# Optimization experiments

Measured on AMD Instinct MI355X. Metric: run time of the kernel, lower is better.

## Reference

```python
import jax, jax.numpy as jnp
import numpy as np

BS, N, IN_F, OUT_F, HEADS = 32, 512, 256, 128, 4
NEG_SLOPE = 0.2


def setup_inputs() -> dict:
    key = jax.random.key(0)
    k1, k2, k3, k4, k5 = jax.random.split(key, 5)
    inputs = jax.random.normal(k1, (BS, N, IN_F), dtype=jnp.float32)
    adj = (jax.random.uniform(k2, (BS, N, N)) > 0.5).astype(jnp.float32)
    # xavier_normal-style init with relu gain sqrt(2)
    w = jax.random.normal(k3, (IN_F, HEADS * OUT_F), dtype=jnp.float32) * (
        np.sqrt(2.0) * np.sqrt(2.0 / (IN_F + HEADS * OUT_F))
    )
    a_i = jax.random.normal(k4, (HEADS, OUT_F, 1), dtype=jnp.float32) * (
        np.sqrt(2.0) * np.sqrt(2.0 / (OUT_F + 1))
    )
    a_j = jax.random.normal(k5, (HEADS, OUT_F, 1), dtype=jnp.float32) * (
        np.sqrt(2.0) * np.sqrt(2.0 / (OUT_F + 1))
    )
    bias = jnp.zeros((HEADS * OUT_F,), dtype=jnp.float32)
    return {"inputs": inputs, "adj": adj, "w": w, "a_i": a_i, "a_j": a_j, "bias": bias}


def reference(inputs, adj, w, a_i, a_j, bias):
    bs, n, _ = inputs.shape
    H, D = a_i.shape[0], a_i.shape[1]
    # self_loop_type == 2: adjacency unchanged
    # project: [bs, n, H, D]
    h = jnp.matmul(inputs, w).reshape(bs, n, H, D)
    # additive attention coefficients: [bs, n, H]
    coeff_i = jnp.einsum('bnhd,hdo->bnho', h, a_i)[..., 0]
    coeff_j = jnp.einsum('bnhd,hdo->bnho', h, a_j)[..., 0]
    # broadcast-sum scores e[b, i, j, h], leaky relu
    e = jax.nn.leaky_relu(coeff_i[:, :, None, :] + coeff_j[:, None, :, :],
                          negative_slope=NEG_SLOPE)
    adj_h = adj[..., None]  # [bs, n, n, 1], broadcasts over heads
    masked_e = jnp.where(adj_h <= 0, jnp.float32(-1e9), e)
    # softmax over neighbor axis j (dim 2), then re-mask
    attention = jax.nn.softmax(masked_e, axis=2) * adj_h
    # dropout = 0.0 -> no-op; normalize=False, average=False
    # per-head aggregation, all heads at once: out[b,i,h,d] = sum_j att[b,i,j,h] h[b,j,h,d]
    out = jnp.einsum('bijh,bjhd->bihd', attention, h).reshape(bs, n, H * D)
    return out + bias
```

## Files before the change

### kernel.cpp

```cpp
#include <hip/hip_runtime.h>

#define BSZ 32
#define NN 512
#define INF 256
#define NH 4
#define HD 512
#define NEG_SLOPE 0.2f

typedef __attribute__((ext_vector_type(8))) short bf16x8;
typedef __attribute__((ext_vector_type(8))) unsigned short ushort8;
typedef __attribute__((ext_vector_type(4))) float f32x4;

static __device__ __forceinline__ unsigned short f2bf(float f) {
    unsigned u = __builtin_bit_cast(unsigned, f);
    return (unsigned short)((u + 0x7FFFu + ((u >> 16) & 1u)) >> 16);
}

static __device__ __forceinline__ bf16x8 pk8(float4 a, float4 b) {
    unsigned d0, d1, d2, d3;
    asm("v_cvt_pk_bf16_f32 %0, %1, %2" : "=v"(d0) : "v"(a.x), "v"(a.y));
    asm("v_cvt_pk_bf16_f32 %0, %1, %2" : "=v"(d1) : "v"(a.z), "v"(a.w));
    asm("v_cvt_pk_bf16_f32 %0, %1, %2" : "=v"(d2) : "v"(b.x), "v"(b.y));
    asm("v_cvt_pk_bf16_f32 %0, %1, %2" : "=v"(d3) : "v"(b.z), "v"(b.w));
    uint4 u; u.x = d0; u.y = d1; u.z = d2; u.w = d3;
    return __builtin_bit_cast(bf16x8, u);
}

static __device__ __forceinline__ void gl_lds16(const void* g, void* l) {
    __builtin_amdgcn_global_load_lds(
        (const __attribute__((address_space(1))) unsigned int*)g,
        (__attribute__((address_space(3))) unsigned int*)l, 16, 0, 0);
}

__global__ __launch_bounds__(256) void k_prep(
    const float* __restrict__ w, unsigned short* __restrict__ wB,
    const float* __restrict__ adj, unsigned char* __restrict__ mbB)
{
    const int bid = blockIdx.x;
    if (bid < 2048) {
        const int swz = (bid & 7) * 256 + (bid >> 3);
        const int lane = threadIdx.x & 63, wave = threadIdx.x >> 6;
        const int row0 = swz * 8 + wave * 2;
        #pragma unroll
        for (int rr = 0; rr < 2; ++rr) {
            const float* ap = adj + (size_t)(row0 + rr) * NN + lane * 8;
            float4 a0 = *(const float4*)ap;
            float4 a1 = *(const float4*)(ap + 4);
            unsigned byte = 0;
            byte |= (a0.x > 0.f) ? 1u : 0u;  byte |= (a0.y > 0.f) ? 2u : 0u;
            byte |= (a0.z > 0.f) ? 4u : 0u;  byte |= (a0.w > 0.f) ? 8u : 0u;
            byte |= (a1.x > 0.f) ? 16u : 0u; byte |= (a1.y > 0.f) ? 32u : 0u;
            byte |= (a1.z > 0.f) ? 64u : 0u; byte |= (a1.w > 0.f) ? 128u : 0u;
            mbB[(size_t)(row0 + rr) * 64 + lane] = (unsigned char)byte;
        }
    } else {
        int gid = (bid - 2048) * 256 + threadIdx.x;
        int c = gid & 511, k = gid >> 9;
        int kb = k >> 5, g = (k >> 3) & 3, e = k & 7;
        wB[(((size_t)(kb * 4 + g) * 512) + c) * 8 + e] = f2bf(w[(size_t)k * 512 + c]);
    }
}

__global__ __launch_bounds__(256) void k_proj(
    const float* __restrict__ x, const unsigned short* __restrict__ wB,
    const float* __restrict__ ai, const float* __restrict__ aj,
    unsigned short* __restrict__ hB, float* __restrict__ ciT, float* __restrict__ cjT)
{
    __shared__ unsigned short hs[NH * 4096];
    const int tid = threadIdx.x;
    const int lane = tid & 63, head = tid >> 6;
    const int l15 = lane & 15, g = lane >> 4;
    const int orig = blockIdx.x;
    const int swz = (orig & 7) * 64 + (orig >> 3);
    const int row0 = swz * 32;

    f32x4 acc[2][8] = {};
    const float* xp0 = x + (size_t)(row0 + l15) * INF + g * 8;
    const float* xp1 = xp0 + 16 * INF;
    const unsigned short* bp = wB + ((size_t)g * 512 + head * 128 + l15) * 8;

    #pragma unroll
    for (int kb = 0; kb < 8; ++kb) {
        float4 f0 = *(const float4*)(xp0 + kb * 32);
        float4 f1 = *(const float4*)(xp0 + kb * 32 + 4);
        float4 f2 = *(const float4*)(xp1 + kb * 32);
        float4 f3 = *(const float4*)(xp1 + kb * 32 + 4);
        bf16x8 a0 = pk8(f0, f1);
        bf16x8 a1 = pk8(f2, f3);
        #pragma unroll
        for (int nf = 0; nf < 8; ++nf) {
            bf16x8 bv = *(const bf16x8*)(bp + (size_t)kb * 16384 + nf * 128);
            acc[0][nf] = __builtin_amdgcn_mfma_f32_16x16x32_bf16(a0, bv, acc[0][nf], 0, 0, 0);
            acc[1][nf] = __builtin_amdgcn_mfma_f32_16x16x32_bf16(a1, bv, acc[1][nf], 0, 0, 0);
        }
    }

    float aiv[8], ajv[8];
    #pragma unroll
    for (int nf = 0; nf < 8; ++nf) {
        aiv[nf] = ai[head * 128 + nf * 16 + l15];
        ajv[nf] = aj[head * 128 + nf * 16 + l15];
    }
    const int b = row0 >> 9;
    const int nloc0 = row0 & 511;
    const int kb2 = nloc0 >> 5;

    #pragma unroll
    for (int m = 0; m < 2; ++m) {
        float pi[4] = {0,0,0,0}, pj[4] = {0,0,0,0};
        #pragma unroll
        for (int nf = 0; nf < 8; ++nf)
            #pragma unroll
            for (int reg = 0; reg < 4; ++reg) {
                pi[reg] = fmaf(acc[m][nf][reg], aiv[nf], pi[reg]);
                pj[reg] = fmaf(acc[m][nf][reg], ajv[nf], pj[reg]);
            }
        #pragma unroll
        for (int reg = 0; reg < 4; ++reg) {
            #pragma unroll
            for (int off = 1; off < 16; off <<= 1) {
                pi[reg] += __shfl_xor(pi[reg], off);
                pj[reg] += __shfl_xor(pj[reg], off);
            }
        }
        if (l15 == 0) {
            #pragma unroll
            for (int reg = 0; reg < 4; ++reg) {
                int n = nloc0 + 16 * m + 4 * g + reg;
                ciT[((size_t)(head * BSZ + b) * NN) + n] = pi[reg];
                cjT[((size_t)(head * BSZ + b) * NN) + n] = pj[reg];
            }
        }
        #pragma unroll
        for (int reg = 0; reg < 4; ++reg) {
            int jloc = 16 * m + 4 * g + reg;
            int g2 = jloc >> 3, e = jloc & 7;
            #pragma unroll
            for (int nf = 0; nf < 8; ++nf)
                hs[head * 4096 + nf * 512 + g2 * 128 + l15 * 8 + e] =
                    f2bf(acc[m][nf][reg]);
        }
    }
    __syncthreads();
    {
        ushort8* dst = (ushort8*)(hB + (((size_t)(b * 4 + head) * 16 + kb2) * 4096));
        const ushort8* src = (const ushort8*)(hs + head * 4096);
        #pragma unroll
        for (int it = 0; it < 8; ++it)
            dst[it * 64 + lane] = src[it * 64 + lane];
    }
}

__global__ __launch_bounds__(256, 4) void k_attn(
    const unsigned short* __restrict__ hB, const float* __restrict__ ciT,
    const float* __restrict__ cjT, const unsigned* __restrict__ mb,
    const float* __restrict__ bias, float* __restrict__ out)
{
    __shared__ __align__(16) unsigned short Bst[2][4096];
    __shared__ __align__(16) float cjh[NN];
    __shared__ float cih[64];
    __shared__ unsigned maskS[64][17];
    __shared__ float Mpart[4];

    const int tid = threadIdx.x;
    const int lane = tid & 63, wave = tid >> 6;
    const int l15 = lane & 15, g = lane >> 4;

    const int orig = blockIdx.x;
    const int swz = (orig & 7) * 128 + (orig >> 3);
    const int b  = swz >> 5;
    const int h  = (swz >> 3) & 3;
    const int i0 = (swz & 7) * 64;

    const char* gslab = (const char*)(hB + (size_t)(b * NH + h) * 65536);

    gl_lds16(gslab + wave * 2048 + lane * 16,        (char*)&Bst[0][0] + wave * 2048);
    gl_lds16(gslab + wave * 2048 + 1024 + lane * 16, (char*)&Bst[0][0] + wave * 2048 + 1024);

    {
        const float* src = cjT + (size_t)(h * BSZ + b) * NN;
        float v0 = src[tid], v1 = src[tid + 256];
        cjh[tid] = v0; cjh[tid + 256] = v1;
        float mv = fmaxf(v0, v1);
        #pragma unroll
        for (int off = 32; off; off >>= 1) mv = fmaxf(mv, __shfl_xor(mv, off));
        if (lane == 0) Mpart[wave] = mv;
        if (tid < 64) cih[tid] = ciT[(size_t)(h * BSZ + b) * NN + i0 + tid];
        uint4 m4 = ((const uint4*)(mb + ((size_t)b * NN + i0) * 16))[tid];
        int base = tid * 4, row = base >> 4, wi = base & 15;
        maskS[row][wi] = m4.x; maskS[row][wi + 1] = m4.y;
        maskS[row][wi + 2] = m4.z; maskS[row][wi + 3] = m4.w;
    }
    __syncthreads();

    const float M = fmaxf(fmaxf(Mpart[0], Mpart[1]), fmaxf(Mpart[2], Mpart[3]));
    const float bc = cih[wave * 16 + l15];
    float smx = bc + M;
    const float mrow = fmaxf(smx, NEG_SLOPE * smx);

    float bvv[8];
    #pragma unroll
    for (int nf = 0; nf < 8; ++nf) bvv[nf] = bias[h * 128 + nf * 16 + l15];

    bf16x8 ones;
    #pragma unroll
    for (int e = 0; e < 8; ++e) ones[e] = (short)0x3F80;

    f32x4 acc[8] = {};
    f32x4 accs = {};
    int cur = 0;
    const unsigned* mrowp = maskS[wave * 16 + l15];

    for (int kb = 0; kb < 16; ++kb) {
        if (kb < 15) {
            const char* gs = gslab + (size_t)(kb + 1) * 8192 + wave * 2048 + lane * 16;
            char* ld = (char*)&Bst[cur ^ 1][0] + wave * 2048;
            gl_lds16(gs, ld);
            gl_lds16(gs + 1024, ld + 1024);
        }

        float4 cva = *(const float4*)&cjh[kb * 32 + g * 8];
        float4 cvb = *(const float4*)&cjh[kb * 32 + g * 8 + 4];
        float cj8[8] = {cva.x, cva.y, cva.z, cva.w, cvb.x, cvb.y, cvb.z, cvb.w};
        unsigned byte = (mrowp[kb] >> (g * 8)) & 0xFFu;
        float p[8];
        #pragma unroll
        for (int e = 0; e < 8; ++e) {
            float s = bc + cj8[e];
            s = fmaxf(s, NEG_SLOPE * s);
            float pe = __expf(s - mrow);
            p[e] = ((byte >> e) & 1u) ? pe : 0.f;
        }
        unsigned d0, d1, d2, d3;
        asm("v_cvt_pk_bf16_f32 %0, %1, %2" : "=v"(d0) : "v"(p[0]), "v"(p[1]));
        asm("v_cvt_pk_bf16_f32 %0, %1, %2" : "=v"(d1) : "v"(p[2]), "v"(p[3]));
        asm("v_cvt_pk_bf16_f32 %0, %1, %2" : "=v"(d2) : "v"(p[4]), "v"(p[5]));
        asm("v_cvt_pk_bf16_f32 %0, %1, %2" : "=v"(d3) : "v"(p[6]), "v"(p[7]));
        uint4 u; u.x = d0; u.y = d1; u.z = d2; u.w = d3;
        bf16x8 av = __builtin_bit_cast(bf16x8, u);

        const char* bb = (const char*)&Bst[cur][0] + lane * 16;
        bf16x8 bfr[8];
        #pragma unroll
        for (int nf = 0; nf < 8; ++nf)
            bfr[nf] = *(const bf16x8*)(bb + nf * 1024);

        #pragma unroll
        for (int nf = 0; nf < 8; ++nf)
            acc[nf] = __builtin_amdgcn_mfma_f32_16x16x32_bf16(av, bfr[nf], acc[nf], 0, 0, 0);
        accs = __builtin_amdgcn_mfma_f32_16x16x32_bf16(av, ones, accs, 0, 0, 0);

        if (kb < 15) { __syncthreads(); cur ^= 1; }
    }

    #pragma unroll
    for (int reg = 0; reg < 4; ++reg) {
        float sum = accs[reg];
        float inv = sum > 0.f ? 1.f / sum : 0.f;
        const int i = i0 + wave * 16 + g * 4 + reg;
        #pragma unroll
        for (int nf = 0; nf < 8; ++nf) {
            int colg = h * 128 + nf * 16 + l15;
            out[(size_t)(b * NN + i) * HD + colg] = acc[nf][reg] * inv + bvv[nf];
        }
    }
}

extern "C" void kernel_launch(void* const* d_in, const int* in_sizes, int n_in,
                              void* d_out, int out_size, void* d_ws, size_t ws_size,
                              hipStream_t stream)
{
    const float* x    = (const float*)d_in[0];
    const float* adj  = (const float*)d_in[1];
    const float* w    = (const float*)d_in[2];
    const float* ai   = (const float*)d_in[3];
    const float* aj   = (const float*)d_in[4];
    const float* bias = (const float*)d_in[5];
    float* out = (float*)d_out;

    char* ws = (char*)d_ws;
    unsigned short* wB = (unsigned short*)ws;
    unsigned short* hB = (unsigned short*)(ws + 262144);
    float* ciT         = (float*)(ws + 17039360);
    float* cjT         = (float*)(ws + 17301504);
    unsigned char* mbB = (unsigned char*)(ws + 17563648);

    k_prep<<<2560, 256, 0, stream>>>(w, wB, adj, mbB);
    k_proj<<<BSZ * NN / 32, 256, 0, stream>>>(x, wB, ai, aj, hB, ciT, cjT);
    k_attn<<<BSZ * NH * (NN / 64), 256, 0, stream>>>(hB, ciT, cjT,
                                                     (const unsigned*)mbB, bias, out);
}
```

Before: 53.70 us.

## Load attention value tiles directly into registers instead of LDS double buffer

The attention kernel no longer stages each 8 KB value tile of h into a shared-memory double buffer with global_load_lds and per-iteration barriers. Each wave now loads the full tile straight from global memory into a register double buffer (bcur/bnxt), which removes the __syncthreads and the LDS reads. The cost is four times more global/L2 load traffic per block, since every wave fetches the whole tile, plus extra VGPR pressure. Separately, the block-index swizzles in the prep and projection kernels are dropped, and the bias is read in the epilogue rather than preloaded into registers.

```diff
diff --git a/kernel.cpp b/kernel.cpp
--- a/kernel.cpp
+++ b/kernel.cpp
@@ -26,21 +26,14 @@
     return __builtin_bit_cast(bf16x8, u);
 }
 
-static __device__ __forceinline__ void gl_lds16(const void* g, void* l) {
-    __builtin_amdgcn_global_load_lds(
-        (const __attribute__((address_space(1))) unsigned int*)g,
-        (__attribute__((address_space(3))) unsigned int*)l, 16, 0, 0);
-}
-
 __global__ __launch_bounds__(256) void k_prep(
     const float* __restrict__ w, unsigned short* __restrict__ wB,
     const float* __restrict__ adj, unsigned char* __restrict__ mbB)
 {
     const int bid = blockIdx.x;
     if (bid < 2048) {
-        const int swz = (bid & 7) * 256 + (bid >> 3);
         const int lane = threadIdx.x & 63, wave = threadIdx.x >> 6;
-        const int row0 = swz * 8 + wave * 2;
+        const int row0 = bid * 8 + wave * 2;
         #pragma unroll
         for (int rr = 0; rr < 2; ++rr) {
             const float* ap = adj + (size_t)(row0 + rr) * NN + lane * 8;
@@ -70,9 +63,7 @@
     const int tid = threadIdx.x;
     const int lane = tid & 63, head = tid >> 6;
     const int l15 = lane & 15, g = lane >> 4;
-    const int orig = blockIdx.x;
-    const int swz = (orig & 7) * 64 + (orig >> 3);
-    const int row0 = swz * 32;
+    const int row0 = blockIdx.x * 32;
 
     f32x4 acc[2][8] = {};
     const float* xp0 = x + (size_t)(row0 + l15) * INF + g * 8;
@@ -156,7 +147,6 @@
     const float* __restrict__ cjT, const unsigned* __restrict__ mb,
     const float* __restrict__ bias, float* __restrict__ out)
 {
-    __shared__ __align__(16) unsigned short Bst[2][4096];
     __shared__ __align__(16) float cjh[NN];
     __shared__ float cih[64];
     __shared__ unsigned maskS[64][17];
@@ -171,11 +161,6 @@
     const int b  = swz >> 5;
     const int h  = (swz >> 3) & 3;
     const int i0 = (swz & 7) * 64;
-
-    const char* gslab = (const char*)(hB + (size_t)(b * NH + h) * 65536);
-
-    gl_lds16(gslab + wave * 2048 + lane * 16,        (char*)&Bst[0][0] + wave * 2048);
-    gl_lds16(gslab + wave * 2048 + 1024 + lane * 16, (char*)&Bst[0][0] + wave * 2048 + 1024);
 
     {
         const float* src = cjT + (size_t)(h * BSZ + b) * NN;
@@ -198,25 +183,27 @@
     float smx = bc + M;
     const float mrow = fmaxf(smx, NEG_SLOPE * smx);
 
-    float bvv[8];
-    #pragma unroll
-    for (int nf = 0; nf < 8; ++nf) bvv[nf] = bias[h * 128 + nf * 16 + l15];
-
     bf16x8 ones;
     #pragma unroll
     for (int e = 0; e < 8; ++e) ones[e] = (short)0x3F80;
 
     f32x4 acc[8] = {};
     f32x4 accs = {};
-    int cur = 0;
     const unsigned* mrowp = maskS[wave * 16 + l15];
-
+    const char* base = (const char*)hB + (size_t)(b * NH + h) * 131072 + lane * 16;
+
+    bf16x8 bcur[8], bnxt[8];
+    #pragma unroll
+    for (int nf = 0; nf < 8; ++nf)
+        bcur[nf] = *(const bf16x8*)(base + nf * 1024);
+
+    #pragma unroll 2
     for (int kb = 0; kb < 16; ++kb) {
         if (kb < 15) {
-            const char* gs = gslab + (size_t)(kb + 1) * 8192 + wave * 2048 + lane * 16;
-            char* ld = (char*)&Bst[cur ^ 1][0] + wave * 2048;
-            gl_lds16(gs, ld);
-            gl_lds16(gs + 1024, ld + 1024);
+            const char* nb = base + (size_t)(kb + 1) * 8192;
+            #pragma unroll
+            for (int nf = 0; nf < 8; ++nf)
+                bnxt[nf] = *(const bf16x8*)(nb + nf * 1024);
         }
 
         float4 cva = *(const float4*)&cjh[kb * 32 + g * 8];
@@ -239,18 +226,13 @@
         uint4 u; u.x = d0; u.y = d1; u.z = d2; u.w = d3;
         bf16x8 av = __builtin_bit_cast(bf16x8, u);
 
-        const char* bb = (const char*)&Bst[cur][0] + lane * 16;
-        bf16x8 bfr[8];
         #pragma unroll
         for (int nf = 0; nf < 8; ++nf)
-            bfr[nf] = *(const bf16x8*)(bb + nf * 1024);
-
-        #pragma unroll
-        for (int nf = 0; nf < 8; ++nf)
-            acc[nf] = __builtin_amdgcn_mfma_f32_16x16x32_bf16(av, bfr[nf], acc[nf], 0, 0, 0);
+            acc[nf] = __builtin_amdgcn_mfma_f32_16x16x32_bf16(av, bcur[nf], acc[nf], 0, 0, 0);
         accs = __builtin_amdgcn_mfma_f32_16x16x32_bf16(av, ones, accs, 0, 0, 0);
 
-        if (kb < 15) { __syncthreads(); cur ^= 1; }
+        #pragma unroll
+        for (int nf = 0; nf < 8; ++nf) bcur[nf] = bnxt[nf];
     }
 
     #pragma unroll
@@ -261,7 +243,8 @@
         #pragma unroll
         for (int nf = 0; nf < 8; ++nf) {
             int colg = h * 128 + nf * 16 + l15;
-            out[(size_t)(b * NN + i) * HD + colg] = acc[nf][reg] * inv + bvv[nf];
+            out[(size_t)(b * NN + i) * HD + colg] =
+                acc[nf][reg] * inv + bias[colg];
         }
     }
 }
```

After: 52.01 us. 1.03x faster.

## Process 128 query rows per attention block to reuse staged h tiles

Applied to the files above, without the earlier changes.

Each attention block now handles 128 query rows instead of 64, with every wave computing two 16-row tiles. Each B fragment read from LDS therefore feeds two MFMAs, halving the global loads of the h slab and the LDS reads per output. The grid shrinks to 512 blocks and launch bounds drop to 2 blocks per CU to leave room for the doubled accumulators, which lowers occupancy. The XCD block swizzles are also removed from the prep and projection kernels.

```diff
diff --git a/kernel.cpp b/kernel.cpp
--- a/kernel.cpp
+++ b/kernel.cpp
@@ -38,9 +38,8 @@
 {
     const int bid = blockIdx.x;
     if (bid < 2048) {
-        const int swz = (bid & 7) * 256 + (bid >> 3);
         const int lane = threadIdx.x & 63, wave = threadIdx.x >> 6;
-        const int row0 = swz * 8 + wave * 2;
+        const int row0 = bid * 8 + wave * 2;
         #pragma unroll
         for (int rr = 0; rr < 2; ++rr) {
             const float* ap = adj + (size_t)(row0 + rr) * NN + lane * 8;
@@ -70,9 +69,7 @@
     const int tid = threadIdx.x;
     const int lane = tid & 63, head = tid >> 6;
     const int l15 = lane & 15, g = lane >> 4;
-    const int orig = blockIdx.x;
-    const int swz = (orig & 7) * 64 + (orig >> 3);
-    const int row0 = swz * 32;
+    const int row0 = blockIdx.x * 32;
 
     f32x4 acc[2][8] = {};
     const float* xp0 = x + (size_t)(row0 + l15) * INF + g * 8;
@@ -151,15 +148,15 @@
     }
 }
 
-__global__ __launch_bounds__(256, 4) void k_attn(
+__global__ __launch_bounds__(256, 2) void k_attn(
     const unsigned short* __restrict__ hB, const float* __restrict__ ciT,
     const float* __restrict__ cjT, const unsigned* __restrict__ mb,
     const float* __restrict__ bias, float* __restrict__ out)
 {
     __shared__ __align__(16) unsigned short Bst[2][4096];
     __shared__ __align__(16) float cjh[NN];
-    __shared__ float cih[64];
-    __shared__ unsigned maskS[64][17];
+    __shared__ float cih[128];
+    __shared__ unsigned maskS[128][17];
     __shared__ float Mpart[4];
 
     const int tid = threadIdx.x;
@@ -167,10 +164,10 @@
     const int l15 = lane & 15, g = lane >> 4;
 
     const int orig = blockIdx.x;
-    const int swz = (orig & 7) * 128 + (orig >> 3);
-    const int b  = swz >> 5;
-    const int h  = (swz >> 3) & 3;
-    const int i0 = (swz & 7) * 64;
+    const int swz = (orig & 7) * 64 + (orig >> 3);
+    const int b  = swz >> 4;
+    const int h  = (swz >> 2) & 3;
+    const int i0 = (swz & 3) * 128;
 
     const char* gslab = (const char*)(hB + (size_t)(b * NH + h) * 65536);
 
@@ -185,18 +182,25 @@
         #pragma unroll
         for (int off = 32; off; off >>= 1) mv = fmaxf(mv, __shfl_xor(mv, off));
         if (lane == 0) Mpart[wave] = mv;
-        if (tid < 64) cih[tid] = ciT[(size_t)(h * BSZ + b) * NN + i0 + tid];
-        uint4 m4 = ((const uint4*)(mb + ((size_t)b * NN + i0) * 16))[tid];
-        int base = tid * 4, row = base >> 4, wi = base & 15;
-        maskS[row][wi] = m4.x; maskS[row][wi + 1] = m4.y;
-        maskS[row][wi + 2] = m4.z; maskS[row][wi + 3] = m4.w;
+        if (tid < 128) cih[tid] = ciT[(size_t)(h * BSZ + b) * NN + i0 + tid];
+        const uint4* m4p = (const uint4*)(mb + ((size_t)b * NN + i0) * 16);
+        #pragma unroll
+        for (int it = 0; it < 2; ++it) {
+            int idx = tid + it * 256;
+            uint4 m4 = m4p[idx];
+            int base = idx * 4, row = base >> 4, wi = base & 15;
+            maskS[row][wi] = m4.x; maskS[row][wi + 1] = m4.y;
+            maskS[row][wi + 2] = m4.z; maskS[row][wi + 3] = m4.w;
+        }
     }
     __syncthreads();
 
     const float M = fmaxf(fmaxf(Mpart[0], Mpart[1]), fmaxf(Mpart[2], Mpart[3]));
-    const float bc = cih[wave * 16 + l15];
-    float smx = bc + M;
-    const float mrow = fmaxf(smx, NEG_SLOPE * smx);
+    const float bc0 = cih[wave * 16 + l15];
+    const float bc1 = cih[64 + wave * 16 + l15];
+    float s0 = bc0 + M, s1 = bc1 + M;
+    const float mrow0 = fmaxf(s0, NEG_SLOPE * s0);
+    const float mrow1 = fmaxf(s1, NEG_SLOPE * s1);
 
     float bvv[8];
     #pragma unroll
@@ -206,10 +210,11 @@
     #pragma unroll
     for (int e = 0; e < 8; ++e) ones[e] = (short)0x3F80;
 
-    f32x4 acc[8] = {};
-    f32x4 accs = {};
+    f32x4 acc0[8] = {}, acc1[8] = {};
+    f32x4 accs0 = {}, accs1 = {};
     int cur = 0;
-    const unsigned* mrowp = maskS[wave * 16 + l15];
+    const unsigned* mrowp0 = maskS[wave * 16 + l15];
+    const unsigned* mrowp1 = maskS[64 + wave * 16 + l15];
 
     for (int kb = 0; kb < 16; ++kb) {
         if (kb < 15) {
@@ -222,46 +227,60 @@
         float4 cva = *(const float4*)&cjh[kb * 32 + g * 8];
         float4 cvb = *(const float4*)&cjh[kb * 32 + g * 8 + 4];
         float cj8[8] = {cva.x, cva.y, cva.z, cva.w, cvb.x, cvb.y, cvb.z, cvb.w};
-        unsigned byte = (mrowp[kb] >> (g * 8)) & 0xFFu;
-        float p[8];
+
+        unsigned byte0 = (mrowp0[kb] >> (g * 8)) & 0xFFu;
+        unsigned byte1 = (mrowp1[kb] >> (g * 8)) & 0xFFu;
+        float p0[8], p1[8];
         #pragma unroll
         for (int e = 0; e < 8; ++e) {
-            float s = bc + cj8[e];
-            s = fmaxf(s, NEG_SLOPE * s);
-            float pe = __expf(s - mrow);
-            p[e] = ((byte >> e) & 1u) ? pe : 0.f;
-        }
-        unsigned d0, d1, d2, d3;
-        asm("v_cvt_pk_bf16_f32 %0, %1, %2" : "=v"(d0) : "v"(p[0]), "v"(p[1]));
-        asm("v_cvt_pk_bf16_f32 %0, %1, %2" : "=v"(d1) : "v"(p[2]), "v"(p[3]));
-        asm("v_cvt_pk_bf16_f32 %0, %1, %2" : "=v"(d2) : "v"(p[4]), "v"(p[5]));
-        asm("v_cvt_pk_bf16_f32 %0, %1, %2" : "=v"(d3) : "v"(p[6]), "v"(p[7]));
-        uint4 u; u.x = d0; u.y = d1; u.z = d2; u.w = d3;
-        bf16x8 av = __builtin_bit_cast(bf16x8, u);
+            float sa = bc0 + cj8[e];
+            sa = fmaxf(sa, NEG_SLOPE * sa);
+            float pa = __expf(sa - mrow0);
+            p0[e] = ((byte0 >> e) & 1u) ? pa : 0.f;
+            float sb = bc1 + cj8[e];
+            sb = fmaxf(sb, NEG_SLOPE * sb);
+            float pb = __expf(sb - mrow1);
+            p1[e] = ((byte1 >> e) & 1u) ? pb : 0.f;
+        }
+        unsigned d0, d1, d2, d3, e0, e1, e2, e3;
+        asm("v_cvt_pk_bf16_f32 %0, %1, %2" : "=v"(d0) : "v"(p0[0]), "v"(p0[1]));
+        asm("v_cvt_pk_bf16_f32 %0, %1, %2" : "=v"(d1) : "v"(p0[2]), "v"(p0[3]));
+        asm("v_cvt_pk_bf16_f32 %0, %1, %2" : "=v"(d2) : "v"(p0[4]), "v"(p0[5]));
+        asm("v_cvt_pk_bf16_f32 %0, %1, %2" : "=v"(d3) : "v"(p0[6]), "v"(p0[7]));
+        asm("v_cvt_pk_bf16_f32 %0, %1, %2" : "=v"(e0) : "v"(p1[0]), "v"(p1[1]));
+        asm("v_cvt_pk_bf16_f32 %0, %1, %2" : "=v"(e1) : "v"(p1[2]), "v"(p1[3]));
+        asm("v_cvt_pk_bf16_f32 %0, %1, %2" : "=v"(e2) : "v"(p1[4]), "v"(p1[5]));
+        asm("v_cvt_pk_bf16_f32 %0, %1, %2" : "=v"(e3) : "v"(p1[6]), "v"(p1[7]));
+        uint4 u0; u0.x = d0; u0.y = d1; u0.z = d2; u0.w = d3;
+        uint4 u1; u1.x = e0; u1.y = e1; u1.z = e2; u1.w = e3;
+        bf16x8 av0 = __builtin_bit_cast(bf16x8, u0);
+        bf16x8 av1 = __builtin_bit_cast(bf16x8, u1);
 
         const char* bb = (const char*)&Bst[cur][0] + lane * 16;
-        bf16x8 bfr[8];
-        #pragma unroll
-        for (int nf = 0; nf < 8; ++nf)
-            bfr[nf] = *(const bf16x8*)(bb + nf * 1024);
-
-        #pragma unroll
-        for (int nf = 0; nf < 8; ++nf)
-            acc[nf] = __builtin_amdgcn_mfma_f32_16x16x32_bf16(av, bfr[nf], acc[nf], 0, 0, 0);
-        accs = __builtin_amdgcn_mfma_f32_16x16x32_bf16(av, ones, accs, 0, 0, 0);
+        #pragma unroll
+        for (int nf = 0; nf < 8; ++nf) {
+            bf16x8 bv = *(const bf16x8*)(bb + nf * 1024);
+            acc0[nf] = __builtin_amdgcn_mfma_f32_16x16x32_bf16(av0, bv, acc0[nf], 0, 0, 0);
+            acc1[nf] = __builtin_amdgcn_mfma_f32_16x16x32_bf16(av1, bv, acc1[nf], 0, 0, 0);
+        }
+        accs0 = __builtin_amdgcn_mfma_f32_16x16x32_bf16(av0, ones, accs0, 0, 0, 0);
+        accs1 = __builtin_amdgcn_mfma_f32_16x16x32_bf16(av1, ones, accs1, 0, 0, 0);
 
         if (kb < 15) { __syncthreads(); cur ^= 1; }
     }
 
     #pragma unroll
     for (int reg = 0; reg < 4; ++reg) {
-        float sum = accs[reg];
-        float inv = sum > 0.f ? 1.f / sum : 0.f;
-        const int i = i0 + wave * 16 + g * 4 + reg;
+        float sum0 = accs0[reg], sum1 = accs1[reg];
+        float inv0 = sum0 > 0.f ? 1.f / sum0 : 0.f;
+        float inv1 = sum1 > 0.f ? 1.f / sum1 : 0.f;
+        const int ia = i0 + wave * 16 + g * 4 + reg;
+        const int ib = ia + 64;
         #pragma unroll
         for (int nf = 0; nf < 8; ++nf) {
             int colg = h * 128 + nf * 16 + l15;
-            out[(size_t)(b * NN + i) * HD + colg] = acc[nf][reg] * inv + bvv[nf];
+            out[(size_t)(b * NN + ia) * HD + colg] = acc0[nf][reg] * inv0 + bvv[nf];
+            out[(size_t)(b * NN + ib) * HD + colg] = acc1[nf][reg] * inv1 + bvv[nf];
         }
     }
 }
@@ -287,6 +306,6 @@
 
     k_prep<<<2560, 256, 0, stream>>>(w, wB, adj, mbB);
     k_proj<<<BSZ * NN / 32, 256, 0, stream>>>(x, wB, ai, aj, hB, ciT, cjT);
-    k_attn<<<BSZ * NH * (NN / 64), 256, 0, stream>>>(hB, ciT, cjT,
-                                                     (const unsigned*)mbB, bias, out);
-}
+    k_attn<<<BSZ * NH * (NN / 128), 256, 0, stream>>>(hB, ciT, cjT,
+                                                      (const unsigned*)mbB, bias, out);
+}
```

New measurement: 50.75 us. 5.5% less time.

## Split attention output columns across two blocks and drop block swizzles

Applied to the files above, without the earlier changes.

The attention kernel now splits each head's 128 output columns into two halves handled by separate blocks. This doubles the grid, halves the per-block LDS staging and accumulators, and raises the occupancy hint from 4 to 8. The aim is more parallelism and better latency hiding. In exchange, each block recomputes the softmax weights and row sums for its half, so that exp/mask work is duplicated. The XCD-style block swizzles in the prep and projection kernels are also removed, which changes how their memory accesses are spread across chiplets.

```diff
diff --git a/kernel.cpp b/kernel.cpp
--- a/kernel.cpp
+++ b/kernel.cpp
@@ -38,9 +38,8 @@
 {
     const int bid = blockIdx.x;
     if (bid < 2048) {
-        const int swz = (bid & 7) * 256 + (bid >> 3);
         const int lane = threadIdx.x & 63, wave = threadIdx.x >> 6;
-        const int row0 = swz * 8 + wave * 2;
+        const int row0 = bid * 8 + wave * 2;
         #pragma unroll
         for (int rr = 0; rr < 2; ++rr) {
             const float* ap = adj + (size_t)(row0 + rr) * NN + lane * 8;
@@ -70,9 +69,7 @@
     const int tid = threadIdx.x;
     const int lane = tid & 63, head = tid >> 6;
     const int l15 = lane & 15, g = lane >> 4;
-    const int orig = blockIdx.x;
-    const int swz = (orig & 7) * 64 + (orig >> 3);
-    const int row0 = swz * 32;
+    const int row0 = blockIdx.x * 32;
 
     f32x4 acc[2][8] = {};
     const float* xp0 = x + (size_t)(row0 + l15) * INF + g * 8;
@@ -151,12 +148,12 @@
     }
 }
 
-__global__ __launch_bounds__(256, 4) void k_attn(
+__global__ __launch_bounds__(256, 8) void k_attn(
     const unsigned short* __restrict__ hB, const float* __restrict__ ciT,
     const float* __restrict__ cjT, const unsigned* __restrict__ mb,
     const float* __restrict__ bias, float* __restrict__ out)
 {
-    __shared__ __align__(16) unsigned short Bst[2][4096];
+    __shared__ __align__(16) unsigned short Bst[2][2048];
     __shared__ __align__(16) float cjh[NN];
     __shared__ float cih[64];
     __shared__ unsigned maskS[64][17];
@@ -167,15 +164,17 @@
     const int l15 = lane & 15, g = lane >> 4;
 
     const int orig = blockIdx.x;
-    const int swz = (orig & 7) * 128 + (orig >> 3);
-    const int b  = swz >> 5;
-    const int h  = (swz >> 3) & 3;
-    const int i0 = (swz & 7) * 64;
-
-    const char* gslab = (const char*)(hB + (size_t)(b * NH + h) * 65536);
-
-    gl_lds16(gslab + wave * 2048 + lane * 16,        (char*)&Bst[0][0] + wave * 2048);
-    gl_lds16(gslab + wave * 2048 + 1024 + lane * 16, (char*)&Bst[0][0] + wave * 2048 + 1024);
+    const int swz = (orig & 7) * 256 + (orig >> 3);
+    const int b    = swz >> 6;
+    const int rem  = swz & 63;
+    const int h    = rem >> 4;
+    const int i0   = ((rem >> 1) & 7) * 64;
+    const int half = rem & 1;
+
+    const char* gslab = (const char*)(hB + (size_t)(b * NH + h) * 65536)
+                        + half * 4096;
+
+    gl_lds16(gslab + tid * 16, (char*)&Bst[0][0] + wave * 1024);
 
     {
         const float* src = cjT + (size_t)(h * BSZ + b) * NN;
@@ -198,25 +197,24 @@
     float smx = bc + M;
     const float mrow = fmaxf(smx, NEG_SLOPE * smx);
 
-    float bvv[8];
-    #pragma unroll
-    for (int nf = 0; nf < 8; ++nf) bvv[nf] = bias[h * 128 + nf * 16 + l15];
+    float bvv[4];
+    #pragma unroll
+    for (int nf = 0; nf < 4; ++nf)
+        bvv[nf] = bias[h * 128 + (half * 4 + nf) * 16 + l15];
 
     bf16x8 ones;
     #pragma unroll
     for (int e = 0; e < 8; ++e) ones[e] = (short)0x3F80;
 
-    f32x4 acc[8] = {};
+    f32x4 acc[4] = {};
     f32x4 accs = {};
     int cur = 0;
     const unsigned* mrowp = maskS[wave * 16 + l15];
 
     for (int kb = 0; kb < 16; ++kb) {
         if (kb < 15) {
-            const char* gs = gslab + (size_t)(kb + 1) * 8192 + wave * 2048 + lane * 16;
-            char* ld = (char*)&Bst[cur ^ 1][0] + wave * 2048;
-            gl_lds16(gs, ld);
-            gl_lds16(gs + 1024, ld + 1024);
+            gl_lds16(gslab + (size_t)(kb + 1) * 8192 + tid * 16,
+                     (char*)&Bst[cur ^ 1][0] + wave * 1024);
         }
 
         float4 cva = *(const float4*)&cjh[kb * 32 + g * 8];
@@ -240,14 +238,11 @@
         bf16x8 av = __builtin_bit_cast(bf16x8, u);
 
         const char* bb = (const char*)&Bst[cur][0] + lane * 16;
-        bf16x8 bfr[8];
-        #pragma unroll
-        for (int nf = 0; nf < 8; ++nf)
-            bfr[nf] = *(const bf16x8*)(bb + nf * 1024);
-
-        #pragma unroll
-        for (int nf = 0; nf < 8; ++nf)
-            acc[nf] = __builtin_amdgcn_mfma_f32_16x16x32_bf16(av, bfr[nf], acc[nf], 0, 0, 0);
+        #pragma unroll
+        for (int nf = 0; nf < 4; ++nf) {
+            bf16x8 bv = *(const bf16x8*)(bb + nf * 1024);
+            acc[nf] = __builtin_amdgcn_mfma_f32_16x16x32_bf16(av, bv, acc[nf], 0, 0, 0);
+        }
         accs = __builtin_amdgcn_mfma_f32_16x16x32_bf16(av, ones, accs, 0, 0, 0);
 
         if (kb < 15) { __syncthreads(); cur ^= 1; }
@@ -259,8 +254,8 @@
         float inv = sum > 0.f ? 1.f / sum : 0.f;
         const int i = i0 + wave * 16 + g * 4 + reg;
         #pragma unroll
-        for (int nf = 0; nf < 8; ++nf) {
-            int colg = h * 128 + nf * 16 + l15;
+        for (int nf = 0; nf < 4; ++nf) {
+            int colg = h * 128 + (half * 4 + nf) * 16 + l15;
             out[(size_t)(b * NN + i) * HD + colg] = acc[nf][reg] * inv + bvv[nf];
         }
     }
@@ -287,6 +282,6 @@
 
     k_prep<<<2560, 256, 0, stream>>>(w, wB, adj, mbB);
     k_proj<<<BSZ * NN / 32, 256, 0, stream>>>(x, wB, ai, aj, hB, ciT, cjT);
-    k_attn<<<BSZ * NH * (NN / 64), 256, 0, stream>>>(hB, ciT, cjT,
-                                                     (const unsigned*)mbB, bias, out);
-}
+    k_attn<<<BSZ * NH * (NN / 64) * 2, 256, 0, stream>>>(hB, ciT, cjT,
+                                                         (const unsigned*)mbB, bias, out);
+}
```

Result: slower. 56.89 us (+5.9%).
